# Kernel optimization log

Measured on AMD Instinct MI355X. Metric: run time of the kernel, lower is better.

## Reference

```python
import math
import jax, jax.numpy as jnp
import numpy as np

H = 16          # n_heads
WIN = 512       # window_size (causal, one-sided)
BS = 64         # block_size


def setup_inputs() -> dict:
    key = jax.random.key(0)
    ks = jax.random.split(key, 5)
    B, T, D = 2, 4096, 1024
    x = jax.random.normal(ks[0], (B, T, D), dtype=jnp.float32)
    init = 0.02
    Wq = jax.random.normal(ks[1], (D, D), dtype=jnp.float32) * init
    Wk = jax.random.normal(ks[2], (D, D), dtype=jnp.float32) * init
    Wv = jax.random.normal(ks[3], (D, D), dtype=jnp.float32) * init
    Wo = jax.random.normal(ks[4], (D, D), dtype=jnp.float32) * init
    return {"x": x, "Wq": Wq, "Wk": Wk, "Wv": Wv, "Wo": Wo}


def _sliding_window_attn(q, k, v):
    """Causal sliding-window attention, banded/block-sparse form.

    q,k,v: (B, H, T, hd). Only key blocks within the window of each query
    block are gathered, honoring the sparsity the torch mask encodes.
    """
    B, Hn, T, hd = q.shape
    nb = T // BS                   # number of blocks
    nw1 = WIN // BS + 1            # key blocks touching a query block
    scale = 1.0 / math.sqrt(hd)

    qb = q.reshape(B, Hn, nb, BS, hd)
    kb = k.reshape(B, Hn, nb, BS, hd)
    vb = v.reshape(B, Hn, nb, BS, hd)

    offs = jnp.arange(-(WIN // BS), 1)                 # (nw1,)
    idx_raw = jnp.arange(nb)[:, None] + offs[None, :]  # (nb, nw1)
    idx = jnp.clip(idx_raw, 0, nb - 1)

    kg = jnp.take(kb, idx, axis=2)   # (B,H,nb,nw1,BS,hd)
    vg = jnp.take(vb, idx, axis=2)

    scores = jnp.einsum('bhnqd,bhnwkd->bhnqwk', qb, kg) * scale

    qpos = (jnp.arange(nb) * BS)[:, None, None, None] + jnp.arange(BS)[None, :, None, None]  # (nb,BS,1,1)
    kpos = (idx_raw * BS)[:, None, :, None] + jnp.arange(BS)[None, None, None, :]            # (nb,1,nw1,BS)
    valid = (idx_raw[:, None, :, None] >= 0) & (kpos <= qpos) & (qpos - kpos < WIN)
    scores = jnp.where(valid[None, None], scores, -1e9)

    p = jax.nn.softmax(scores.reshape(B, Hn, nb, BS, nw1 * BS), axis=-1)
    p = p.reshape(B, Hn, nb, BS, nw1, BS)
    out = jnp.einsum('bhnqwk,bhnwkd->bhnqd', p, vg)
    return out.reshape(B, Hn, T, hd)


def reference(x, Wq, Wk, Wv, Wo):
    B, T, D = x.shape
    hd = D // H

    def proj(W):  # torch Linear: x @ W.T
        return (x @ W.T).reshape(B, T, H, hd).transpose(0, 2, 1, 3)

    q, k, v = proj(Wq), proj(Wk), proj(Wv)
    out = _sliding_window_attn(q, k, v)            # (B,H,T,hd)
    out = out.transpose(0, 2, 1, 3).reshape(B, T, D)
    return out @ Wo.T
```

## Files before the change

kernel.cpp:

```cpp
#include <hip/hip_runtime.h>

#define DI static __device__ __forceinline__

typedef __attribute__((ext_vector_type(8))) short short8;
typedef __attribute__((ext_vector_type(4))) float f32x4;

DI unsigned short f2bf(float f) {
    union { float f; unsigned int u; } v; v.f = f;
    unsigned int r = v.u + 0x7FFFu + ((v.u >> 16) & 1u);
    return (unsigned short)(r >> 16);
}

DI void gload_lds16(const void* g, void* l) {
    __builtin_amdgcn_global_load_lds(
        (const __attribute__((address_space(1))) void*)g,
        (__attribute__((address_space(3))) void*)l, 16, 0, 0);
}

DI short8 ldsfrag(const void* base, int row, int bytecol) {
    return *(const short8*)((const char*)base + row * 128 + (bytecol ^ ((row & 7) << 4)));
}

__global__ __launch_bounds__(256) void k_cvt(
    const float* __restrict__ x, const float* __restrict__ wq,
    const float* __restrict__ wk, const float* __restrict__ wv,
    const float* __restrict__ wo,
    unsigned short* __restrict__ xb, unsigned short* __restrict__ wqb,
    unsigned short* __restrict__ wkb, unsigned short* __restrict__ wvb,
    unsigned short* __restrict__ wob)
{
    const float* src; unsigned short* dst; int n;
    switch (blockIdx.y) {
        case 0:  src = x;  dst = xb;  n = 8388608; break;
        case 1:  src = wq; dst = wqb; n = 1048576; break;
        case 2:  src = wk; dst = wkb; n = 1048576; break;
        case 3:  src = wv; dst = wvb; n = 1048576; break;
        default: src = wo; dst = wob; n = 1048576; break;
    }
    int idx = (blockIdx.x * 256 + threadIdx.x) * 4;
    if (idx >= n) return;
    float4 v = *(const float4*)(src + idx);
    unsigned long long o = (unsigned long long)f2bf(v.x)
        | ((unsigned long long)f2bf(v.y) << 16)
        | ((unsigned long long)f2bf(v.z) << 32)
        | ((unsigned long long)f2bf(v.w) << 48);
    *(unsigned long long*)(dst + idx) = o;
}

DI void gemm_tile(const unsigned short* __restrict__ A,
                  const unsigned short* __restrict__ Bw,
                  int m0, int n0, f32x4 acc[4][4],
                  unsigned short* As, unsigned short* Bs)
{
    const int t = threadIdx.x, lane = t & 63;
    const int wid = t >> 6, wr = wid >> 1, wc = wid & 1;
    const int kl = lane & 15, hi = lane >> 4;
#pragma unroll
    for (int mi = 0; mi < 4; ++mi)
#pragma unroll
        for (int ni = 0; ni < 4; ++ni)
            acc[mi][ni] = f32x4{0.f, 0.f, 0.f, 0.f};

    const int c0 = t, c1 = t + 256;
    const int ar0 = m0 + (c0 >> 2), ar1 = m0 + (c1 >> 2);
    const int br0 = n0 + (c0 >> 2), br1 = n0 + (c1 >> 2);
    const int ko0 = (c0 & 3) * 8,   ko1 = (c1 & 3) * 8;

    for (int ks = 0; ks < 1024; ks += 32) {
        __syncthreads();
        gload_lds16(A  + ar0 * 1024 + ks + ko0, As + c0 * 8);
        gload_lds16(A  + ar1 * 1024 + ks + ko1, As + c1 * 8);
        gload_lds16(Bw + br0 * 1024 + ks + ko0, Bs + c0 * 8);
        gload_lds16(Bw + br1 * 1024 + ks + ko1, Bs + c1 * 8);
        __syncthreads();
        short8 a[4], b[4];
#pragma unroll
        for (int mi = 0; mi < 4; ++mi)
            a[mi] = *(const short8*)(As + (wr * 64 + mi * 16 + kl) * 32 + hi * 8);
#pragma unroll
        for (int ni = 0; ni < 4; ++ni)
            b[ni] = *(const short8*)(Bs + (wc * 64 + ni * 16 + kl) * 32 + hi * 8);
#pragma unroll
        for (int mi = 0; mi < 4; ++mi)
#pragma unroll
            for (int ni = 0; ni < 4; ++ni)
                acc[mi][ni] = __builtin_amdgcn_mfma_f32_16x16x32_bf16(
                    a[mi], b[ni], acc[mi][ni], 0, 0, 0);
    }
}

__global__ __launch_bounds__(256) void k_gemm_qkv(
    const unsigned short* __restrict__ xb,
    const unsigned short* __restrict__ wqb, const unsigned short* __restrict__ wkb,
    const unsigned short* __restrict__ wvb,
    unsigned short* __restrict__ Qo, unsigned short* __restrict__ Ko,
    unsigned short* __restrict__ Vo)
{
    __shared__ unsigned short As[4096], Bs[4096];
    const int bx = blockIdx.x, by = blockIdx.y;
    const int w = by >> 3, nb8 = by & 7;
    const unsigned short* Bw = (w == 0) ? wqb : ((w == 1) ? wkb : wvb);
    unsigned short* Ow = (w == 0) ? Qo : ((w == 1) ? Ko : Vo);
    const float sc = (w == 0) ? 0.125f : 1.0f;
    const int m0 = bx * 128, n0 = nb8 * 128;
    f32x4 acc[4][4];
    gemm_tile(xb, Bw, m0, n0, acc, As, Bs);

    const int t = threadIdx.x, lane = t & 63, wid = t >> 6;
    const int wr = wid >> 1, wc = wid & 1, kl = lane & 15, hi = lane >> 4;
    const int h = nb8 * 2 + wc;
    const int bi = bx >> 5;
#pragma unroll
    for (int mi = 0; mi < 4; ++mi)
#pragma unroll
        for (int r = 0; r < 4; ++r) {
            int grow = m0 + wr * 64 + mi * 16 + hi * 4 + r;
            int tt = grow & 4095;
            unsigned short* rowp = Ow + ((long)(bi * 16 + h) * 4096 + tt) * 64;
#pragma unroll
            for (int ni = 0; ni < 4; ++ni)
                rowp[ni * 16 + kl] = f2bf(acc[mi][ni][r] * sc);
        }
}

__global__ __launch_bounds__(256) void k_vtrans(const unsigned short* __restrict__ V,
                                                unsigned short* __restrict__ VT)
{
    __shared__ unsigned short S[64 * 64];
    const int t = threadIdx.x;
    const int bh = blockIdx.y, tb = blockIdx.x;
    const unsigned short* src = V + ((long)bh * 4096 + tb * 64) * 64;
    unsigned short* dst = VT + (long)bh * 4096 * 64 + tb * 64;
    char* sb = (char*)S;
#pragma unroll
    for (int c = t; c < 512; c += 256) {
        int r = c >> 3, o8 = (c & 7) * 8;
        *(uint4*)(sb + r * 128 + ((o8 * 2) ^ (((r >> 3) & 7) << 4))) =
            *(const uint4*)(src + r * 64 + o8);
    }
    __syncthreads();
#pragma unroll
    for (int c = t; c < 512; c += 256) {
        int d = c >> 3, t0 = (c & 7) * 8;
        uint4 val;
        unsigned short* pv = (unsigned short*)&val;
#pragma unroll
        for (int jj = 0; jj < 8; ++jj) {
            int row = t0 + jj;
            pv[jj] = *(const unsigned short*)(sb + row * 128 +
                        ((d * 2) ^ (((row >> 3) & 7) << 4)));
        }
        *(uint4*)(dst + (long)d * 4096 + t0) = val;
    }
}

__global__ __launch_bounds__(256) void k_attn(
    const unsigned short* __restrict__ Q, const unsigned short* __restrict__ K,
    const unsigned short* __restrict__ VT, unsigned short* __restrict__ AO)
{
    __shared__ unsigned short Qs[4096];
    __shared__ unsigned short Ks[2][4096], Vs[2][4096];
    const int t = threadIdx.x, lane = t & 63, wid = t >> 6;
    const int kl = lane & 15, hi = lane >> 4;
    const int bid = blockIdx.x;
    const int sid = (bid & 7) * 256 + (bid >> 3);
    const int i = sid & 63, bh = sid >> 6;
    const int b = bh >> 4, h = bh & 15;
    const char* qg = (const char*)(Q + ((long)bh * 4096 + i * 64) * 64);
    const char* kg = (const char*)(K + (long)bh * 4096 * 64);
    const char* vg = (const char*)(VT + (long)bh * 64 * 4096);

    const int c0 = t, c1 = t + 256;
    const int r0 = c0 >> 3, sw0 = ((c0 & 7) * 16) ^ ((r0 & 7) << 4);
    const int r1 = c1 >> 3, sw1 = ((c1 & 7) * 16) ^ ((r1 & 7) << 4);
    const char* kg0 = kg + r0 * 128 + sw0;
    const char* kg1 = kg + r1 * 128 + sw1;
    const char* vg0 = vg + r0 * 8192 + sw0;
    const char* vg1 = vg + r1 * 8192 + sw1;

    const int j0 = (i >= 8) ? i - 8 : 0;

    gload_lds16(qg + r0 * 128 + sw0, (char*)Qs + c0 * 16);
    gload_lds16(qg + r1 * 128 + sw1, (char*)Qs + c1 * 16);
    gload_lds16(kg0 + j0 * 8192, (char*)Ks[0] + c0 * 16);
    gload_lds16(kg1 + j0 * 8192, (char*)Ks[0] + c1 * 16);
    gload_lds16(vg0 + j0 * 128,  (char*)Vs[0] + c0 * 16);
    gload_lds16(vg1 + j0 * 128,  (char*)Vs[0] + c1 * 16);
    __syncthreads();

    short8 aq[2];
    aq[0] = ldsfrag(Qs, wid * 16 + kl, hi * 16);
    aq[1] = ldsfrag(Qs, wid * 16 + kl, 64 + hi * 16);

    float lsum[4] = {0.f, 0.f, 0.f, 0.f};
    f32x4 o[4];
#pragma unroll
    for (int nt = 0; nt < 4; ++nt) o[nt] = f32x4{0.f, 0.f, 0.f, 0.f};

    const int qrow = wid * 16 + hi * 4;
    char* pw = (char*)Qs + wid * 2048;

    for (int j = j0; j <= i; ++j) {
        const int buf = (j - j0) & 1;
        if (j < i) {
            const int nb = buf ^ 1;
            gload_lds16(kg0 + (j + 1) * 8192, (char*)Ks[nb] + c0 * 16);
            gload_lds16(kg1 + (j + 1) * 8192, (char*)Ks[nb] + c1 * 16);
            gload_lds16(vg0 + (j + 1) * 128,  (char*)Vs[nb] + c0 * 16);
            gload_lds16(vg1 + (j + 1) * 128,  (char*)Vs[nb] + c1 * 16);
        }

        f32x4 s[4];
#pragma unroll
        for (int nt = 0; nt < 4; ++nt) {
            s[nt] = f32x4{0.f, 0.f, 0.f, 0.f};
#pragma unroll
            for (int kk = 0; kk < 2; ++kk)
                s[nt] = __builtin_amdgcn_mfma_f32_16x16x32_bf16(
                    aq[kk], ldsfrag(Ks[buf], nt * 16 + kl, kk * 64 + hi * 16),
                    s[nt], 0, 0, 0);
        }

        if (j == i) {
#pragma unroll
            for (int nt = 0; nt < 4; ++nt) {
                int key = nt * 16 + kl;
#pragma unroll
                for (int r = 0; r < 4; ++r)
                    if (key > qrow + r) s[nt][r] = -1e9f;
            }
        } else if (i - j == 8) {
#pragma unroll
            for (int nt = 0; nt < 4; ++nt) {
                int key = nt * 16 + kl;
#pragma unroll
                for (int r = 0; r < 4; ++r)
                    if (key <= qrow + r) s[nt][r] = -1e9f;
            }
        }

#pragma unroll
        for (int nt = 0; nt < 4; ++nt)
#pragma unroll
            for (int r = 0; r < 4; ++r) {
                float p = __expf(s[nt][r]);
                s[nt][r] = p;
                lsum[r] += p;
            }

#pragma unroll
        for (int nt = 0; nt < 4; ++nt)
#pragma unroll
            for (int r = 0; r < 4; ++r) {
                int q = hi * 4 + r;
                int colb = (nt * 16 + kl) * 2;
                *(unsigned short*)(pw + q * 128 + (colb ^ ((q & 7) << 4))) =
                    f2bf(s[nt][r]);
            }

        short8 pa0 = ldsfrag(pw, kl, hi * 16);
        short8 pa1 = ldsfrag(pw, kl, 64 + hi * 16);
#pragma unroll
        for (int nt = 0; nt < 4; ++nt) {
            o[nt] = __builtin_amdgcn_mfma_f32_16x16x32_bf16(
                pa0, ldsfrag(Vs[buf], nt * 16 + kl, hi * 16), o[nt], 0, 0, 0);
            o[nt] = __builtin_amdgcn_mfma_f32_16x16x32_bf16(
                pa1, ldsfrag(Vs[buf], nt * 16 + kl, 64 + hi * 16), o[nt], 0, 0, 0);
        }

        __syncthreads();
    }

#pragma unroll
    for (int d = 1; d < 16; d <<= 1)
#pragma unroll
        for (int r = 0; r < 4; ++r) lsum[r] += __shfl_xor(lsum[r], d);

    float inv[4];
#pragma unroll
    for (int r = 0; r < 4; ++r) inv[r] = 1.0f / lsum[r];
#pragma unroll
    for (int r = 0; r < 4; ++r) {
        int tt = i * 64 + wid * 16 + hi * 4 + r;
        unsigned short* rowp = AO + ((long)(b * 4096 + tt)) * 1024 + h * 64;
#pragma unroll
        for (int nt = 0; nt < 4; ++nt)
            rowp[nt * 16 + kl] = f2bf(o[nt][r] * inv[r]);
    }
}

__global__ __launch_bounds__(256) void k_gemm_out(
    const unsigned short* __restrict__ AO, const unsigned short* __restrict__ wob,
    float* __restrict__ out)
{
    __shared__ unsigned short As[4096], Bs[4096];
    f32x4 acc[4][4];
    const int m0 = blockIdx.x * 128, n0 = blockIdx.y * 128;
    gemm_tile(AO, wob, m0, n0, acc, As, Bs);
    const int t = threadIdx.x, lane = t & 63, wid = t >> 6;
    const int wr = wid >> 1, wc = wid & 1, kl = lane & 15, hi = lane >> 4;
#pragma unroll
    for (int mi = 0; mi < 4; ++mi)
#pragma unroll
        for (int r = 0; r < 4; ++r) {
            int grow = m0 + wr * 64 + mi * 16 + hi * 4 + r;
            float* rowp = out + (long)grow * 1024 + n0 + wc * 64;
#pragma unroll
            for (int ni = 0; ni < 4; ++ni)
                rowp[ni * 16 + kl] = acc[mi][ni][r];
        }
}

extern "C" void kernel_launch(void* const* d_in, const int* in_sizes, int n_in,
                              void* d_out, int out_size, void* d_ws, size_t ws_size,
                              hipStream_t stream) {
    const float* x  = (const float*)d_in[0];
    const float* wq = (const float*)d_in[1];
    const float* wk = (const float*)d_in[2];
    const float* wv = (const float*)d_in[3];
    const float* wo = (const float*)d_in[4];

    char* ws = (char*)d_ws;
    const size_t MB = 1024 * 1024;
    unsigned short* xb  = (unsigned short*)(ws);
    unsigned short* wqb = (unsigned short*)(ws + 16 * MB);
    unsigned short* wkb = (unsigned short*)(ws + 18 * MB);
    unsigned short* wvb = (unsigned short*)(ws + 20 * MB);
    unsigned short* wob = (unsigned short*)(ws + 22 * MB);
    unsigned short* Qp  = (unsigned short*)(ws + 24 * MB);
    unsigned short* Kp  = (unsigned short*)(ws + 40 * MB);
    unsigned short* Vp  = (unsigned short*)(ws + 56 * MB);
    unsigned short* VTp = (unsigned short*)(ws + 72 * MB);
    unsigned short* AOp = xb;

    dim3 blk(256);
    k_cvt<<<dim3(8192, 5), blk, 0, stream>>>(x, wq, wk, wv, wo,
                                             xb, wqb, wkb, wvb, wob);
    k_gemm_qkv<<<dim3(64, 24), blk, 0, stream>>>(xb, wqb, wkb, wvb, Qp, Kp, Vp);
    k_vtrans<<<dim3(64, 32), blk, 0, stream>>>(Vp, VTp);
    k_attn<<<2048, blk, 0, stream>>>(Qp, Kp, VTp, AOp);
    k_gemm_out<<<dim3(64, 8), blk, 0, stream>>>(AOp, wob, (float*)d_out);
}
```

Before: 158.1 us.

## Double-buffer GEMM LDS tiles and swizzle shared-memory layout

The shared GEMM tile routine now prefetches the next K-slice into a second LDS buffer while MFMAs run on the current one, with one barrier per iteration instead of two. Global-to-LDS source addresses are XOR-swizzled by row so fragment reads avoid bank conflicts, and reads use the matching swizzle. LDS use per block doubles, which may reduce occupancy.

Result: slower. 168.9 us (+6.8%).

```diff
diff --git a/kernel.cpp b/kernel.cpp
--- a/kernel.cpp
+++ b/kernel.cpp
@@ -19,6 +19,11 @@
 
 DI short8 ldsfrag(const void* base, int row, int bytecol) {
     return *(const short8*)((const char*)base + row * 128 + (bytecol ^ ((row & 7) << 4)));
+}
+
+DI short8 gfrag(const void* base, int row, int hi) {
+    return *(const short8*)((const char*)base + row * 64 +
+                            ((hi ^ ((row >> 1) & 3)) << 4));
 }
 
 __global__ __launch_bounds__(256) void k_cvt(
@@ -62,30 +67,46 @@
             acc[mi][ni] = f32x4{0.f, 0.f, 0.f, 0.f};
 
     const int c0 = t, c1 = t + 256;
-    const int ar0 = m0 + (c0 >> 2), ar1 = m0 + (c1 >> 2);
-    const int br0 = n0 + (c0 >> 2), br1 = n0 + (c1 >> 2);
-    const int ko0 = (c0 & 3) * 8,   ko1 = (c1 & 3) * 8;
-
-    for (int ks = 0; ks < 1024; ks += 32) {
-        __syncthreads();
-        gload_lds16(A  + ar0 * 1024 + ks + ko0, As + c0 * 8);
-        gload_lds16(A  + ar1 * 1024 + ks + ko1, As + c1 * 8);
-        gload_lds16(Bw + br0 * 1024 + ks + ko0, Bs + c0 * 8);
-        gload_lds16(Bw + br1 * 1024 + ks + ko1, Bs + c1 * 8);
-        __syncthreads();
+    const int row0 = c0 >> 2, row1 = c1 >> 2;
+    const int ss0 = ((c0 & 3) ^ ((row0 >> 1) & 3)) * 8;
+    const int ss1 = ((c1 & 3) ^ ((row1 >> 1) & 3)) * 8;
+    const unsigned short* a0 = A  + (long)(m0 + row0) * 1024 + ss0;
+    const unsigned short* a1 = A  + (long)(m0 + row1) * 1024 + ss1;
+    const unsigned short* b0 = Bw + (long)(n0 + row0) * 1024 + ss0;
+    const unsigned short* b1 = Bw + (long)(n0 + row1) * 1024 + ss1;
+
+    gload_lds16(a0, As + c0 * 8);
+    gload_lds16(a1, As + c1 * 8);
+    gload_lds16(b0, Bs + c0 * 8);
+    gload_lds16(b1, Bs + c1 * 8);
+    __syncthreads();
+
+    for (int ks = 0; ks < 32; ++ks) {
+        const int buf = ks & 1;
+        if (ks < 31) {
+            const int off = (buf ^ 1) * 4096;
+            const int kk = (ks + 1) * 32;
+            gload_lds16(a0 + kk, As + off + c0 * 8);
+            gload_lds16(a1 + kk, As + off + c1 * 8);
+            gload_lds16(b0 + kk, Bs + off + c0 * 8);
+            gload_lds16(b1 + kk, Bs + off + c1 * 8);
+        }
+        const unsigned short* Ab = As + buf * 4096;
+        const unsigned short* Bb = Bs + buf * 4096;
         short8 a[4], b[4];
 #pragma unroll
         for (int mi = 0; mi < 4; ++mi)
-            a[mi] = *(const short8*)(As + (wr * 64 + mi * 16 + kl) * 32 + hi * 8);
+            a[mi] = gfrag(Ab, wr * 64 + mi * 16 + kl, hi);
 #pragma unroll
         for (int ni = 0; ni < 4; ++ni)
-            b[ni] = *(const short8*)(Bs + (wc * 64 + ni * 16 + kl) * 32 + hi * 8);
+            b[ni] = gfrag(Bb, wc * 64 + ni * 16 + kl, hi);
 #pragma unroll
         for (int mi = 0; mi < 4; ++mi)
 #pragma unroll
             for (int ni = 0; ni < 4; ++ni)
                 acc[mi][ni] = __builtin_amdgcn_mfma_f32_16x16x32_bf16(
                     a[mi], b[ni], acc[mi][ni], 0, 0, 0);
+        __syncthreads();
     }
 }
 
@@ -96,7 +117,7 @@
     unsigned short* __restrict__ Qo, unsigned short* __restrict__ Ko,
     unsigned short* __restrict__ Vo)
 {
-    __shared__ unsigned short As[4096], Bs[4096];
+    __shared__ unsigned short As[2][4096], Bs[2][4096];
     const int bx = blockIdx.x, by = blockIdx.y;
     const int w = by >> 3, nb8 = by & 7;
     const unsigned short* Bw = (w == 0) ? wqb : ((w == 1) ? wkb : wvb);
@@ -104,7 +125,7 @@
     const float sc = (w == 0) ? 0.125f : 1.0f;
     const int m0 = bx * 128, n0 = nb8 * 128;
     f32x4 acc[4][4];
-    gemm_tile(xb, Bw, m0, n0, acc, As, Bs);
+    gemm_tile(xb, Bw, m0, n0, acc, &As[0][0], &Bs[0][0]);
 
     const int t = threadIdx.x, lane = t & 63, wid = t >> 6;
     const int wr = wid >> 1, wc = wid & 1, kl = lane & 15, hi = lane >> 4;
@@ -293,10 +314,10 @@
     const unsigned short* __restrict__ AO, const unsigned short* __restrict__ wob,
     float* __restrict__ out)
 {
-    __shared__ unsigned short As[4096], Bs[4096];
+    __shared__ unsigned short As[2][4096], Bs[2][4096];
     f32x4 acc[4][4];
     const int m0 = blockIdx.x * 128, n0 = blockIdx.y * 128;
-    gemm_tile(AO, wob, m0, n0, acc, As, Bs);
+    gemm_tile(AO, wob, m0, n0, acc, &As[0][0], &Bs[0][0]);
     const int t = threadIdx.x, lane = t & 63, wid = t >> 6;
     const int wr = wid >> 1, wc = wid & 1, kl = lane & 15, hi = lane >> 4;
 #pragma unroll
```

## Rewrite projection GEMMs as 256x256 triple-buffered tiles with 8 waves

Applied to the files above, without the earlier changes.

Both projection GEMMs now use 256x256 output tiles computed by 512-thread blocks. The K loop streams through a triple-buffered LDS ring with an XOR-swizzled layout, waiting on vmcnt and a single barrier per step instead of two syncthreads, and raises wave priority around the MFMA block. The goal is to hide global-to-LDS load latency, cut barrier overhead and LDS bank conflicts, and improve operand reuse. The cost is higher register pressure, 96KB of dynamic shared memory, and far fewer blocks (128 for the output GEMM), which may underfill the GPU.

New measurement: 158.2 us (median of 2 runs). Within noise of the previous version (+0.1%).

```diff
diff --git a/kernel.cpp b/kernel.cpp
--- a/kernel.cpp
+++ b/kernel.cpp
@@ -47,79 +47,108 @@
     *(unsigned long long*)(dst + idx) = o;
 }
 
-DI void gemm_tile(const unsigned short* __restrict__ A,
-                  const unsigned short* __restrict__ Bw,
-                  int m0, int n0, f32x4 acc[4][4],
-                  unsigned short* As, unsigned short* Bs)
+DI void gemm256_core(const unsigned short* __restrict__ Ag,
+                     const unsigned short* __restrict__ Bg,
+                     int m0, int n0, char* smem, f32x4 acc[8][4])
 {
     const int t = threadIdx.x, lane = t & 63;
-    const int wid = t >> 6, wr = wid >> 1, wc = wid & 1;
+    const int wid = t >> 6, wr = wid >> 2, wc = wid & 3;
     const int kl = lane & 15, hi = lane >> 4;
-#pragma unroll
-    for (int mi = 0; mi < 4; ++mi)
-#pragma unroll
-        for (int ni = 0; ni < 4; ++ni)
-            acc[mi][ni] = f32x4{0.f, 0.f, 0.f, 0.f};
-
-    const int c0 = t, c1 = t + 256;
-    const int ar0 = m0 + (c0 >> 2), ar1 = m0 + (c1 >> 2);
-    const int br0 = n0 + (c0 >> 2), br1 = n0 + (c1 >> 2);
-    const int ko0 = (c0 & 3) * 8,   ko1 = (c1 & 3) * 8;
-
-    for (int ks = 0; ks < 1024; ks += 32) {
-        __syncthreads();
-        gload_lds16(A  + ar0 * 1024 + ks + ko0, As + c0 * 8);
-        gload_lds16(A  + ar1 * 1024 + ks + ko1, As + c1 * 8);
-        gload_lds16(Bw + br0 * 1024 + ks + ko0, Bs + c0 * 8);
-        gload_lds16(Bw + br1 * 1024 + ks + ko1, Bs + c1 * 8);
-        __syncthreads();
-        short8 a[4], b[4];
-#pragma unroll
-        for (int mi = 0; mi < 4; ++mi)
-            a[mi] = *(const short8*)(As + (wr * 64 + mi * 16 + kl) * 32 + hi * 8);
-#pragma unroll
-        for (int ni = 0; ni < 4; ++ni)
-            b[ni] = *(const short8*)(Bs + (wc * 64 + ni * 16 + kl) * 32 + hi * 8);
-#pragma unroll
-        for (int mi = 0; mi < 4; ++mi)
-#pragma unroll
-            for (int ni = 0; ni < 4; ++ni)
-                acc[mi][ni] = __builtin_amdgcn_mfma_f32_16x16x32_bf16(
-                    a[mi], b[ni], acc[mi][ni], 0, 0, 0);
-    }
-}
-
-__global__ __launch_bounds__(256) void k_gemm_qkv(
+
+#pragma unroll
+    for (int m = 0; m < 8; ++m)
+#pragma unroll
+        for (int n = 0; n < 4; ++n)
+            acc[m][n] = f32x4{0.f, 0.f, 0.f, 0.f};
+
+    const int c0 = t, c1 = t + 512;
+    const int r0 = c0 >> 2, r1 = c1 >> 2;
+    const int s0 = ((c0 & 3) ^ ((r0 >> 1) & 3)) * 8;
+    const int s1 = ((c1 & 3) ^ ((r1 >> 1) & 3)) * 8;
+    const unsigned short* pa0 = Ag + (long)(m0 + r0) * 1024 + s0;
+    const unsigned short* pa1 = Ag + (long)(m0 + r1) * 1024 + s1;
+    const unsigned short* pb0 = Bg + (long)(n0 + r0) * 1024 + s0;
+    const unsigned short* pb1 = Bg + (long)(n0 + r1) * 1024 + s1;
+
+#define STAGE(TILE, BUF) do {                                          \
+        char* _sa = smem + (BUF) * 32768;                              \
+        gload_lds16(pa0 + (TILE) * 32, _sa + c0 * 16);                 \
+        gload_lds16(pa1 + (TILE) * 32, _sa + c1 * 16);                 \
+        gload_lds16(pb0 + (TILE) * 32, _sa + 16384 + c0 * 16);         \
+        gload_lds16(pb1 + (TILE) * 32, _sa + 16384 + c1 * 16);         \
+    } while (0)
+
+    STAGE(0, 0);
+    STAGE(1, 1);
+
+    const int swz = ((hi ^ ((kl >> 1) & 3)) << 4);
+    const int aoff = (wr * 128 + kl) * 64 + swz;
+    const int boff = 16384 + (wc * 64 + kl) * 64 + swz;
+
+#define KSTEP(KS, CUR, PRE, ISSUE, VM) do {                                   \
+        asm volatile("s_waitcnt vmcnt(" VM ")" ::: "memory");                 \
+        __builtin_amdgcn_s_barrier();                                         \
+        __builtin_amdgcn_sched_barrier(0);                                    \
+        if (ISSUE) STAGE((KS) + 2, PRE);                                      \
+        const char* _ab = smem + (CUR) * 32768 + aoff;                        \
+        const char* _bb = smem + (CUR) * 32768 + boff;                        \
+        short8 _fa[8], _fb[4];                                                \
+        _Pragma("unroll")                                                     \
+        for (int m = 0; m < 8; ++m) _fa[m] = *(const short8*)(_ab + m * 1024);\
+        _Pragma("unroll")                                                     \
+        for (int n = 0; n < 4; ++n) _fb[n] = *(const short8*)(_bb + n * 1024);\
+        __builtin_amdgcn_s_setprio(1);                                        \
+        _Pragma("unroll")                                                     \
+        for (int m = 0; m < 8; ++m)                                           \
+        _Pragma("unroll")                                                     \
+            for (int n = 0; n < 4; ++n)                                       \
+                acc[m][n] = __builtin_amdgcn_mfma_f32_16x16x32_bf16(          \
+                    _fa[m], _fb[n], acc[m][n], 0, 0, 0);                      \
+        __builtin_amdgcn_s_setprio(0);                                        \
+    } while (0)
+
+    for (int u = 0; u < 10; ++u) {
+        const int ks = u * 3;
+        KSTEP(ks + 0, 0, 2, 1, "4");
+        KSTEP(ks + 1, 1, 0, 1, "4");
+        KSTEP(ks + 2, 2, 1, 1, "4");
+    }
+    KSTEP(30, 0, 2, 0, "4");
+    KSTEP(31, 1, 0, 0, "0");
+#undef KSTEP
+#undef STAGE
+}
+
+__global__ __launch_bounds__(512, 2) void k_gemm_qkv(
     const unsigned short* __restrict__ xb,
     const unsigned short* __restrict__ wqb, const unsigned short* __restrict__ wkb,
     const unsigned short* __restrict__ wvb,
     unsigned short* __restrict__ Qo, unsigned short* __restrict__ Ko,
     unsigned short* __restrict__ Vo)
 {
-    __shared__ unsigned short As[4096], Bs[4096];
+    extern __shared__ char smem[];
     const int bx = blockIdx.x, by = blockIdx.y;
-    const int w = by >> 3, nb8 = by & 7;
+    const int w = by >> 2, nb = by & 3;
     const unsigned short* Bw = (w == 0) ? wqb : ((w == 1) ? wkb : wvb);
     unsigned short* Ow = (w == 0) ? Qo : ((w == 1) ? Ko : Vo);
     const float sc = (w == 0) ? 0.125f : 1.0f;
-    const int m0 = bx * 128, n0 = nb8 * 128;
-    f32x4 acc[4][4];
-    gemm_tile(xb, Bw, m0, n0, acc, As, Bs);
+
+    f32x4 acc[8][4];
+    gemm256_core(xb, Bw, bx * 256, nb * 256, smem, acc);
 
     const int t = threadIdx.x, lane = t & 63, wid = t >> 6;
-    const int wr = wid >> 1, wc = wid & 1, kl = lane & 15, hi = lane >> 4;
-    const int h = nb8 * 2 + wc;
-    const int bi = bx >> 5;
-#pragma unroll
-    for (int mi = 0; mi < 4; ++mi)
+    const int wr = wid >> 2, wc = wid & 3, kl = lane & 15, hi = lane >> 4;
+    const int h = nb * 4 + wc;
+#pragma unroll
+    for (int m = 0; m < 8; ++m)
 #pragma unroll
         for (int r = 0; r < 4; ++r) {
-            int grow = m0 + wr * 64 + mi * 16 + hi * 4 + r;
-            int tt = grow & 4095;
+            int grow = bx * 256 + wr * 128 + m * 16 + hi * 4 + r;
+            int bi = grow >> 12, tt = grow & 4095;
             unsigned short* rowp = Ow + ((long)(bi * 16 + h) * 4096 + tt) * 64;
 #pragma unroll
-            for (int ni = 0; ni < 4; ++ni)
-                rowp[ni * 16 + kl] = f2bf(acc[mi][ni][r] * sc);
+            for (int n = 0; n < 4; ++n)
+                rowp[n * 16 + kl] = f2bf(acc[m][n][r] * sc);
         }
 }
 
@@ -289,25 +318,26 @@
     }
 }
 
-__global__ __launch_bounds__(256) void k_gemm_out(
+__global__ __launch_bounds__(512, 2) void k_gemm_out(
     const unsigned short* __restrict__ AO, const unsigned short* __restrict__ wob,
     float* __restrict__ out)
 {
-    __shared__ unsigned short As[4096], Bs[4096];
-    f32x4 acc[4][4];
-    const int m0 = blockIdx.x * 128, n0 = blockIdx.y * 128;
-    gemm_tile(AO, wob, m0, n0, acc, As, Bs);
+    extern __shared__ char smem[];
+    const int bx = blockIdx.x, nb = blockIdx.y;
+    f32x4 acc[8][4];
+    gemm256_core(AO, wob, bx * 256, nb * 256, smem, acc);
+
     const int t = threadIdx.x, lane = t & 63, wid = t >> 6;
-    const int wr = wid >> 1, wc = wid & 1, kl = lane & 15, hi = lane >> 4;
-#pragma unroll
-    for (int mi = 0; mi < 4; ++mi)
+    const int wr = wid >> 2, wc = wid & 3, kl = lane & 15, hi = lane >> 4;
+#pragma unroll
+    for (int m = 0; m < 8; ++m)
 #pragma unroll
         for (int r = 0; r < 4; ++r) {
-            int grow = m0 + wr * 64 + mi * 16 + hi * 4 + r;
-            float* rowp = out + (long)grow * 1024 + n0 + wc * 64;
-#pragma unroll
-            for (int ni = 0; ni < 4; ++ni)
-                rowp[ni * 16 + kl] = acc[mi][ni][r];
+            int grow = bx * 256 + wr * 128 + m * 16 + hi * 4 + r;
+            float* rowp = out + (long)grow * 1024 + nb * 256 + wc * 64;
+#pragma unroll
+            for (int n = 0; n < 4; ++n)
+                rowp[n * 16 + kl] = acc[m][n][r];
         }
 }
 
@@ -333,11 +363,17 @@
     unsigned short* VTp = (unsigned short*)(ws + 72 * MB);
     unsigned short* AOp = xb;
 
+    hipFuncSetAttribute((const void*)k_gemm_qkv,
+                        hipFuncAttributeMaxDynamicSharedMemorySize, 98304);
+    hipFuncSetAttribute((const void*)k_gemm_out,
+                        hipFuncAttributeMaxDynamicSharedMemorySize, 98304);
+
     dim3 blk(256);
     k_cvt<<<dim3(8192, 5), blk, 0, stream>>>(x, wq, wk, wv, wo,
                                              xb, wqb, wkb, wvb, wob);
-    k_gemm_qkv<<<dim3(64, 24), blk, 0, stream>>>(xb, wqb, wkb, wvb, Qp, Kp, Vp);
+    k_gemm_qkv<<<dim3(32, 12), 512, 98304, stream>>>(xb, wqb, wkb, wvb,
+                                                     Qp, Kp, Vp);
     k_vtrans<<<dim3(64, 32), blk, 0, stream>>>(Vp, VTp);
     k_attn<<<2048, blk, 0, stream>>>(Qp, Kp, VTp, AOp);
-    k_gemm_out<<<dim3(64, 8), blk, 0, stream>>>(AOp, wob, (float*)d_out);
-}
+    k_gemm_out<<<dim3(32, 4), 512, 98304, stream>>>(AOp, wob, (float*)d_out);
+}
```
